# Performance work log

Hardware: AMD Instinct MI355X
Metric: run time of the kernel (lower is better)

Reference implementation:

```python
import jax, jax.numpy as jnp
import numpy as np

B, C, T = 4, 512, 4096
N2 = 32          # d_state // 2 complex modes
H = 2048         # hidden_channels
EPS = 1e-5


def setup_inputs() -> dict:
    key = jax.random.key(0)
    ks = jax.random.split(key, 8)
    dt_min, dt_max = 1e-3, 1e-1
    log_dt = jax.random.uniform(ks[1], (C,)) * (np.log(dt_max) - np.log(dt_min)) + np.log(dt_min)
    return {
        "x": jax.random.normal(ks[0], (B, C, T), jnp.float32),
        # ChannelwiseLayerNorm affine params
        "gamma": jnp.ones((C,), jnp.float32),
        "beta": jnp.zeros((C,), jnp.float32),
        # S4D kernel params (standard S4D-Lin init)
        "log_dt": log_dt.astype(jnp.float32),
        "C_re": jax.random.normal(ks[2], (C, N2), jnp.float32),
        "C_im": jax.random.normal(ks[3], (C, N2), jnp.float32),
        "log_A_real": jnp.log(0.5 * jnp.ones((C, N2), jnp.float32)),
        "A_imag": jnp.tile(jnp.pi * jnp.arange(N2, dtype=jnp.float32), (C, 1)),
        "D": jax.random.normal(ks[4], (C,), jnp.float32),
        # S4D output linear (Conv1d k=1 -> 2C, then GLU over channels)
        "Wo": jax.random.normal(ks[5], (2 * C, C), jnp.float32) / np.sqrt(C),
        "bo": jnp.zeros((2 * C,), jnp.float32),
        # FC MLP: Linear(C->H), PReLU(H), Linear(H->C)
        "W1": jax.random.normal(ks[6], (H, C), jnp.float32) / np.sqrt(C),
        "b1": jnp.zeros((H,), jnp.float32),
        "prelu_a": 0.25 * jnp.ones((H,), jnp.float32),
        "W2": jax.random.normal(ks[7], (C, H), jnp.float32) / np.sqrt(H),
        "b2": jnp.zeros((C,), jnp.float32),
    }


def reference(x, gamma, beta, log_dt, C_re, C_im, log_A_real, A_imag, D,
              Wo, bo, W1, b1, prelu_a, W2, b2):
    # ---- ChannelwiseLayerNorm over the channel dim of [B, C, T] ----
    mean = jnp.mean(x, axis=1, keepdims=True)
    var = jnp.var(x, axis=1, keepdims=True)
    u = gamma[None, :, None] * (x - mean) * jax.lax.rsqrt(var + EPS) + beta[None, :, None]

    # ---- S4D: diagonal SSM kernel via Vandermonde, applied by FFT conv ----
    L = x.shape[-1]
    dt = jnp.exp(log_dt)[:, None]                       # [C, 1]
    A = -jnp.exp(log_A_real) + 1j * A_imag              # [C, N2] complex diag
    dtA = A * dt                                        # [C, N2]
    Cd = (C_re + 1j * C_im) * (jnp.exp(dtA) - 1.0) / A  # discretized C (ZOH)
    vand = jnp.exp(dtA[..., None] * jnp.arange(L, dtype=jnp.float32))  # [C, N2, L]
    K = 2.0 * jnp.einsum('hn,hnl->hl', Cd, vand).real   # [C, L]

    k_f = jnp.fft.rfft(K, n=2 * L)                      # [C, L+1]
    u_f = jnp.fft.rfft(u, n=2 * L)                      # [B, C, L+1]
    y = jnp.fft.irfft(u_f * k_f, n=2 * L)[..., :L]      # causal conv
    y = y + u * D[None, :, None]                        # skip connection
    y = jax.nn.gelu(y, approximate=False)
    # output linear (1x1 conv to 2C) + GLU over channel dim
    z = jnp.einsum('oc,bct->bot', Wo, y) + bo[None, :, None]
    y = z[:, :C] * jax.nn.sigmoid(z[:, C:])             # [B, C, T]

    # ---- FC MLP with PReLU (per hidden channel) ----
    y = y.transpose(0, 2, 1)                            # [B, T, C]
    h = y @ W1.T + b1                                   # [B, T, H]
    h = jnp.where(h >= 0, h, prelu_a * h)
    y = h @ W2.T + b2                                   # [B, T, C]

    return x + y.transpose(0, 2, 1)                     # residual, [B, C, T]
```

## Files before the change

### kernel.cpp

```cpp
#include <hip/hip_runtime.h>
#include <math.h>

#define BB 4
#define CC 512
#define TT 4096
#define NN2 32
#define HH 2048

typedef __bf16 bf8v __attribute__((ext_vector_type(8)));
typedef __bf16 bf4v __attribute__((ext_vector_type(4)));
typedef float  f4v  __attribute__((ext_vector_type(4)));
typedef unsigned short u16x8 __attribute__((ext_vector_type(8)));

__device__ __forceinline__ void gload16(const void* g, void* l){
  __builtin_amdgcn_global_load_lds(
      (const __attribute__((address_space(1))) unsigned int*)g,
      (__attribute__((address_space(3))) unsigned int*)l, 16, 0, 0);
}
__device__ __forceinline__ float fast_gelu(float v){
  float x2 = v*v;
  float x  = 0.7978845608f*v*fmaf(0.044715f, x2, 1.0f);
  float t  = __expf(2.0f*x);
  return v - v*__builtin_amdgcn_rcpf(1.0f + t);
}
__device__ __forceinline__ float fast_sigmoid(float g){
  return __builtin_amdgcn_rcpf(1.0f + __expf(-g));
}
__device__ __forceinline__ unsigned short bfbits(float v){
  __bf16 h = (__bf16)v;
  return __builtin_bit_cast(unsigned short, h);
}

__global__ __launch_bounds__(256) void ln_kernel(
    const float* __restrict__ x, const float* __restrict__ gamma,
    const float* __restrict__ beta, __bf16* __restrict__ u)
{
  int tile = blockIdx.x & (TT/64 - 1);
  int b    = blockIdx.x >> 6;
  int tl = threadIdx.x & 63;
  int cg = threadIdx.x >> 6;
  int t = tile*64 + tl;
  const float* xp = x + (size_t)b*CC*TT + t;
  float s = 0.f, s2 = 0.f;
  #pragma unroll 4
  for (int c = cg*128; c < (cg+1)*128; ++c){
    float v = xp[(size_t)c*TT];
    s += v; s2 = fmaf(v, v, s2);
  }
  __shared__ float ls[4][64], ls2[4][64], mean_s[64], inv_s[64];
  ls[cg][tl] = s; ls2[cg][tl] = s2;
  __syncthreads();
  if (threadIdx.x < 64){
    float ss  = ls [0][tl]+ls [1][tl]+ls [2][tl]+ls [3][tl];
    float ss2 = ls2[0][tl]+ls2[1][tl]+ls2[2][tl]+ls2[3][tl];
    float mean = ss * (1.f/CC);
    float var  = ss2 * (1.f/CC) - mean*mean;
    mean_s[tl] = mean;
    inv_s[tl]  = rsqrtf(var + 1e-5f);
  }
  __syncthreads();
  float mean = mean_s[tl], inv = inv_s[tl];
  __bf16* up = u + (size_t)b*CC*TT + t;
  #pragma unroll 4
  for (int c = cg*128; c < (cg+1)*128; ++c){
    float v = xp[(size_t)c*TT];
    up[(size_t)c*TT] = (__bf16)fmaf(gamma[c]*inv, v - mean, beta[c]);
  }
}

__global__ __launch_bounds__(256) void build_mats(
    const float* __restrict__ log_dt, const float* __restrict__ C_re,
    const float* __restrict__ C_im, const float* __restrict__ log_A_real,
    const float* __restrict__ A_imag, const float* __restrict__ Dp,
    __bf16* __restrict__ Tt, __bf16* __restrict__ V, __bf16* __restrict__ B2)
{
  __shared__ float cpart[4][64][33];
  __shared__ float kk[4][65];
  const int wv = threadIdx.x >> 6, lane = threadIdx.x & 63;
  const int c = blockIdx.x*4 + wv;
  const int m = lane & 31;
  float dt = expf(log_dt[c]);
  float Ar = -expf(log_A_real[c*NN2+m]);
  float Ai = A_imag[c*NN2+m];
  float er = expf(Ar*dt);
  float sw_, cw_; sincosf(Ai*dt, &sw_, &cw_);
  float wre = er*cw_, wim = er*sw_;
  float nr = wre-1.f, ni = wim;
  float inv = 1.f/(Ar*Ar + Ai*Ai);
  float qr = (nr*Ar + ni*Ai)*inv;
  float qi = (ni*Ar - nr*Ai)*inv;
  float Cr = C_re[c*NN2+m], Ci = C_im[c*NN2+m];
  float okr =  2.f*(Cr*qr - Ci*qi);
  float oki = -2.f*(Cr*qi + Ci*qr);
  __bf16* Ttc = Tt + (size_t)c*4096;
  __bf16* Vc  = V  + (size_t)c*4096;
  __bf16* B2c = B2 + (size_t)c*4096;
  if (lane < 32){
    float pre = 1.f, pim = 0.f;
    for (int l = 0; l <= 64; ++l){
      if (l <= 63){
        Vc[(2*m)*64   + (63-l)] = (__bf16)pre;
        Vc[(2*m+1)*64 + (63-l)] = (__bf16)pim;
      }
      float cR = fmaf(okr, pre,  oki*pim);
      float cQ = fmaf(oki, pre, -okr*pim);
      if (l <= 63) cpart[wv][l][m] = cR;
      if (l >= 1){
        B2c[(l-1)*64 + 2*m]   = (__bf16)cR;
        B2c[(l-1)*64 + 2*m+1] = (__bf16)cQ;
      }
      float npre = wre*pre - wim*pim;
      float npim = wre*pim + wim*pre;
      pre = npre; pim = npim;
    }
  }
  __syncthreads();
  float s = 0.f;
  #pragma unroll
  for (int mm = 0; mm < 32; ++mm) s += cpart[wv][lane][mm];
  if (lane == 0) s += Dp[c];
  kk[wv][lane] = s;
  __syncthreads();
  const int n = lane;
  #pragma unroll
  for (int kb = 0; kb < 8; ++kb){
    u16x8 v;
    #pragma unroll
    for (int e = 0; e < 8; ++e){
      int k = kb*8 + e;
      v[e] = bfbits((n >= k) ? kk[wv][n-k] : 0.f);
    }
    *(u16x8*)&Ttc[n*64 + kb*8] = v;
  }
}

__global__ __launch_bounds__(128) void s4dm_kernel(
    const __bf16* __restrict__ u, const float* __restrict__ log_dt,
    const float* __restrict__ log_A_real, const float* __restrict__ A_imag,
    const __bf16* __restrict__ Tt, const __bf16* __restrict__ V,
    const __bf16* __restrict__ B2, __bf16* __restrict__ gout)
{
  __shared__ __align__(16) float gbuf[2][64][66];
  __shared__ __align__(16) unsigned short s0buf[2][64][72];
  const int wv = threadIdx.x >> 6, l = threadIdx.x & 63;
  const int lr = l & 15, q = l >> 4;
  const int seq = blockIdx.x*2 + wv;
  const int c = seq & (CC-1);
  const __bf16* Up  = u  + (size_t)seq*TT;
  const __bf16* Ttc = Tt + (size_t)c*4096;
  const __bf16* Vc  = V  + (size_t)c*4096;
  const __bf16* B2c = B2 + (size_t)c*4096;

  f4v acc[4][4];
  #pragma unroll
  for (int a=0;a<4;++a)
    #pragma unroll
    for (int b=0;b<4;++b)
      #pragma unroll
      for (int r=0;r<4;++r) acc[a][b][r] = 0.f;

  #pragma unroll
  for (int kw = 0; kw < 2; ++kw){
    bf8v af[4], bv[4];
    #pragma unroll
    for (int mt=0;mt<4;++mt)
      af[mt] = *(const bf8v*)(Up + (mt*16+lr)*64 + kw*32 + q*8);
    #pragma unroll
    for (int nt=0;nt<4;++nt)
      bv[nt] = *(const bf8v*)(Vc + (nt*16+lr)*64 + kw*32 + q*8);
    #pragma unroll
    for (int mt=0;mt<4;++mt)
      #pragma unroll
      for (int nt=0;nt<4;++nt)
        acc[mt][nt] = __builtin_amdgcn_mfma_f32_16x16x32_bf16(af[mt], bv[nt], acc[mt][nt], 0,0,0);
  }
  #pragma unroll
  for (int mt=0;mt<4;++mt)
    #pragma unroll
    for (int nt=0;nt<4;++nt)
      #pragma unroll
      for (int r=0;r<4;++r)
        gbuf[wv][mt*16 + q*4 + r][nt*16 + lr] = acc[mt][nt][r];
  __syncthreads();

  if (l < 32){
    const int m = l;
    float dt = expf(log_dt[c]);
    float Ar = -expf(log_A_real[c*NN2+m]);
    float Ai = A_imag[c*NN2+m];
    float er = expf(Ar*dt);
    float sw_, cw_; sincosf(Ai*dt, &sw_, &cw_);
    float wr_ = er*cw_, wi_ = er*sw_;
    #pragma unroll
    for (int sq2=0;sq2<6;++sq2){
      float a=wr_, b=wi_;
      wr_ = a*a - b*b; wi_ = 2.f*a*b;
    }
    float S0r=0.f, S0i=0.f;
    for (int j=0;j<64;++j){
      float gr = gbuf[wv][j][2*m], gi = gbuf[wv][j][2*m+1];
      s0buf[wv][j][2*m]   = bfbits(S0r);
      s0buf[wv][j][2*m+1] = bfbits(S0i);
      float nRe = fmaf(wr_, S0r, fmaf(-wi_, S0i, gr));
      float nIm = fmaf(wr_, S0i, fmaf( wi_, S0r, gi));
      S0r = nRe; S0i = nIm;
    }
  }
  __syncthreads();

  #pragma unroll
  for (int a=0;a<4;++a)
    #pragma unroll
    for (int b=0;b<4;++b)
      #pragma unroll
      for (int r=0;r<4;++r) acc[a][b][r] = 0.f;
  #pragma unroll
  for (int kw = 0; kw < 2; ++kw){
    bf8v af[4], bv[4];
    #pragma unroll
    for (int mt=0;mt<4;++mt)
      af[mt] = *(const bf8v*)(Up + (mt*16+lr)*64 + kw*32 + q*8);
    #pragma unroll
    for (int nt=0;nt<4;++nt)
      bv[nt] = *(const bf8v*)(Ttc + (nt*16+lr)*64 + kw*32 + q*8);
    #pragma unroll
    for (int mt=0;mt<4;++mt)
      #pragma unroll
      for (int nt=0;nt<4;++nt)
        acc[mt][nt] = __builtin_amdgcn_mfma_f32_16x16x32_bf16(af[mt], bv[nt], acc[mt][nt], 0,0,0);
  }
  #pragma unroll
  for (int kw = 0; kw < 2; ++kw){
    bf8v af[4], bv[4];
    #pragma unroll
    for (int mt=0;mt<4;++mt)
      af[mt] = *(const bf8v*)&s0buf[wv][mt*16+lr][kw*32 + q*8];
    #pragma unroll
    for (int nt=0;nt<4;++nt)
      bv[nt] = *(const bf8v*)(B2c + (nt*16+lr)*64 + kw*32 + q*8);
    #pragma unroll
    for (int mt=0;mt<4;++mt)
      #pragma unroll
      for (int nt=0;nt<4;++nt)
        acc[mt][nt] = __builtin_amdgcn_mfma_f32_16x16x32_bf16(af[mt], bv[nt], acc[mt][nt], 0,0,0);
  }
  __syncthreads();

  unsigned short (*ybuf)[72] = (unsigned short(*)[72])&gbuf[wv][0][0];
  #pragma unroll
  for (int mt=0;mt<4;++mt)
    #pragma unroll
    for (int nt=0;nt<4;++nt)
      #pragma unroll
      for (int r=0;r<4;++r)
        ybuf[mt*16 + q*4 + r][nt*16 + lr] = bfbits(fast_gelu(acc[mt][nt][r]));
  __syncthreads();
  u16x8* dst = (u16x8*)(gout + (size_t)seq*TT);
  for (int i = l; i < 512; i += 64){
    int row = i >> 3, cq = i & 7;
    dst[i] = *(const u16x8*)&ybuf[row][cq*8];
  }
}

__global__ __launch_bounds__(256) void tr_kernel(const __bf16* __restrict__ gin,
                                                 __bf16* __restrict__ gout)
{
  __shared__ __align__(16) unsigned short ts[64][72];
  int bt = blockIdx.x;
  int bc = blockIdx.y;
  int b  = blockIdx.z;
  int tid = threadIdx.x;
  const __bf16* gp = gin + ((size_t)b*CC + bc*64)*TT + (size_t)bt*64;
  for (int i = tid; i < 512; i += 256){
    int c = i >> 3, tq = i & 7;
    u16x8 v = *(const u16x8*)(gp + (size_t)c*TT + tq*8);
    #pragma unroll
    for (int s = 0; s < 8; ++s) ts[tq*8+s][c] = v[s];
  }
  __syncthreads();
  __bf16* op = gout + ((size_t)b*TT + bt*64)*CC + bc*64;
  for (int i = tid; i < 512; i += 256){
    int t = i >> 3, cq = i & 7;
    u16x8 v = *(const u16x8*)&ts[t][cq*8];
    *(u16x8*)(op + (size_t)t*CC + cq*8) = v;
  }
}

__global__ __launch_bounds__(256) void cvt_kernel(const float4* __restrict__ in,
                                                  bf4v* __restrict__ out, int n4)
{
  int i = blockIdx.x*256 + threadIdx.x;
  if (i < n4){
    float4 v = in[i];
    bf4v o; o[0]=(__bf16)v.x; o[1]=(__bf16)v.y; o[2]=(__bf16)v.z; o[3]=(__bf16)v.w;
    out[i] = o;
  }
}

template<int MODE>
__global__ __launch_bounds__(512, 2) void mm_kernel(
    const __bf16* __restrict__ Aw, const __bf16* __restrict__ Bt,
    const float* __restrict__ bias, const float* __restrict__ aux,
    void* __restrict__ outp)
{
  constexpr int K  = (MODE==2) ? 2048 : 512;
  constexpr int NT = K/32;
  constexpr int LOGGM = (MODE==1) ? 4 : 2;
  constexpr int GM = 1 << LOGGM;

  __shared__ __align__(16) __bf16 As[2*128*32];
  __shared__ __align__(16) __bf16 Bs[2*256*32];
  __shared__ __align__(16) __bf16 As2[(MODE==0)?2*128*32:8];

  const int bid = blockIdx.x;
  const int X = bid & 7, L = bid >> 3;
  const int m0 = (L & (GM-1)) * 128;
  const int n0 = (X*8 + (L >> LOGGM)) * 256;

  const int tid = threadIdx.x;
  const int l = tid & 63;
  const int lr = l & 15, kh = l >> 4;
  const int w = tid >> 6;
  const int wm = w >> 2, wn = w & 3;
  const int coff = (kh ^ ((lr ^ (lr >> 2)) & 3)) * 16;

  f4v acc[4][4];
  f4v acc2[(MODE==0)?4:1][(MODE==0)?4:1];
  #pragma unroll
  for (int a=0;a<4;++a)
    #pragma unroll
    for (int b=0;b<4;++b)
      #pragma unroll
      for (int r=0;r<4;++r) acc[a][b][r] = 0.f;
  if constexpr (MODE==0){
    #pragma unroll
    for (int a=0;a<4;++a)
      #pragma unroll
      for (int b=0;b<4;++b)
        #pragma unroll
        for (int r=0;r<4;++r) acc2[a][b][r] = 0.f;
  }

  const char* pA  = (const char*)Aw;
  const char* pA2 = (const char*)(Aw + (size_t)CC*K);
  const char* pB  = (const char*)Bt;

  auto stage = [&](int d, int kt){
    {
      int cch = tid;
      int row = cch >> 2;
      int kb = ((cch & 3) ^ ((row ^ (row >> 2)) & 3)) * 16;
      gload16(pA + ((size_t)(m0+row)*K + kt*32)*2 + kb, (char*)As + d*8192 + cch*16);
      if constexpr (MODE==0)
        gload16(pA2 + ((size_t)(m0+row)*K + kt*32)*2 + kb, (char*)As2 + d*8192 + cch*16);
    }
    #pragma unroll
    for (int i=0;i<2;++i){
      int cch = i*512 + tid;
      int row = cch >> 2;
      int kb = ((cch & 3) ^ ((row ^ (row >> 2)) & 3)) * 16;
      gload16(pB + ((size_t)(n0+row)*K + kt*32)*2 + kb, (char*)Bs + d*16384 + cch*16);
    }
  };

  auto compute = [&](int d){
    bf8v af[4], bv4[4];
    #pragma unroll
    for (int mi=0;mi<4;++mi){
      int row = wm*64 + mi*16 + lr;
      af[mi] = *(const bf8v*)((const char*)As + d*8192 + row*64 + coff);
    }
    #pragma unroll
    for (int ni=0;ni<4;++ni){
      int row = wn*64 + ni*16 + lr;
      bv4[ni] = *(const bf8v*)((const char*)Bs + d*16384 + row*64 + coff);
    }
    if constexpr (MODE==0){
      bf8v af2[4];
      #pragma unroll
      for (int mi=0;mi<4;++mi){
        int row = wm*64 + mi*16 + lr;
        af2[mi] = *(const bf8v*)((const char*)As2 + d*8192 + row*64 + coff);
      }
      #pragma unroll
      for (int mi=0;mi<4;++mi)
        #pragma unroll
        for (int ni=0;ni<4;++ni){
          acc [mi][ni] = __builtin_amdgcn_mfma_f32_16x16x32_bf16(af [mi], bv4[ni], acc [mi][ni], 0,0,0);
          acc2[mi][ni] = __builtin_amdgcn_mfma_f32_16x16x32_bf16(af2[mi], bv4[ni], acc2[mi][ni], 0,0,0);
        }
    } else {
      #pragma unroll
      for (int mi=0;mi<4;++mi)
        #pragma unroll
        for (int ni=0;ni<4;++ni)
          acc[mi][ni] = __builtin_amdgcn_mfma_f32_16x16x32_bf16(af[mi], bv4[ni], acc[mi][ni], 0,0,0);
    }
  };

  stage(0, 0);
  __syncthreads();
  int cur = 0;
  #pragma unroll 1
  for (int kt = 1; kt < NT; ++kt){
    stage(cur ^ 1, kt);
    compute(cur);
    __syncthreads();
    cur ^= 1;
  }
  compute(cur);

  if constexpr (MODE==0 || MODE==1){
    const int COUT = (MODE==0) ? CC : HH;
    __bf16* O = (__bf16*)outp;
    #pragma unroll
    for (int mi=0;mi<4;++mi){
      int m = m0 + wm*64 + mi*16 + kh*4;
      float4 bi = *(const float4*)&bias[m];
      float bia[4] = {bi.x, bi.y, bi.z, bi.w};
      float gta[4], paa[4];
      if constexpr (MODE==0){
        float4 bg = *(const float4*)&bias[CC + m];
        gta[0]=bg.x; gta[1]=bg.y; gta[2]=bg.z; gta[3]=bg.w;
      } else {
        float4 pa = *(const float4*)&aux[m];
        paa[0]=pa.x; paa[1]=pa.y; paa[2]=pa.z; paa[3]=pa.w;
      }
      #pragma unroll
      for (int ni=0;ni<4;++ni){
        int tok = n0 + wn*64 + ni*16 + lr;
        bf4v o;
        #pragma unroll
        for (int r=0;r<4;++r){
          float v = acc[mi][ni][r] + bia[r];
          if constexpr (MODE==0){
            float gate = acc2[mi][ni][r] + gta[r];
            v = v * fast_sigmoid(gate);
          } else {
            v = (v >= 0.f) ? v : paa[r]*v;
          }
          o[r] = (__bf16)v;
        }
        *(bf4v*)&O[(size_t)tok*COUT + m] = o;
      }
    }
  } else {
    float* O = (float*)outp;
    #pragma unroll
    for (int mi=0;mi<4;++mi){
      int chb = m0 + wm*64 + mi*16 + kh*4;
      float4 bi = *(const float4*)&bias[chb];
      float bia[4] = {bi.x, bi.y, bi.z, bi.w};
      #pragma unroll
      for (int ni=0;ni<4;++ni){
        int tok = n0 + wn*64 + ni*16 + lr;
        int b = tok >> 12, t = tok & 4095;
        size_t rb = ((size_t)(b*CC + chb))*TT + t;
        #pragma unroll
        for (int r=0;r<4;++r)
          O[rb + (size_t)r*TT] = acc[mi][ni][r] + bia[r] + aux[rb + (size_t)r*TT];
      }
    }
  }
}

extern "C" void kernel_launch(void* const* d_in, const int* in_sizes, int n_in,
                              void* d_out, int out_size, void* d_ws, size_t ws_size,
                              hipStream_t stream)
{
  const float* x          = (const float*)d_in[0];
  const float* gamma      = (const float*)d_in[1];
  const float* beta       = (const float*)d_in[2];
  const float* log_dt     = (const float*)d_in[3];
  const float* C_re       = (const float*)d_in[4];
  const float* C_im       = (const float*)d_in[5];
  const float* log_A_real = (const float*)d_in[6];
  const float* A_imag     = (const float*)d_in[7];
  const float* Dp         = (const float*)d_in[8];
  const float* Wo         = (const float*)d_in[9];
  const float* bo         = (const float*)d_in[10];
  const float* W1         = (const float*)d_in[11];
  const float* b1         = (const float*)d_in[12];
  const float* prelu_a    = (const float*)d_in[13];
  const float* W2         = (const float*)d_in[14];
  const float* b2         = (const float*)d_in[15];
  float* out = (float*)d_out;

  char* base = (char*)d_ws;
  const size_t SEGB = (size_t)BB*CC*TT*2;
  __bf16* u_bf  = (__bf16*)(base);
  __bf16* glu   = (__bf16*)(base);
  __bf16* g_cm  = (__bf16*)(base + SEGB);
  __bf16* g_tm  = (__bf16*)(base + 2*SEGB);
  __bf16* h     = (__bf16*)(base + SEGB);
  __bf16* Tt_all = (__bf16*)(base + 2*SEGB);
  __bf16* V_all  = Tt_all + (size_t)CC*4096;
  __bf16* B2_all = V_all  + (size_t)CC*4096;
  __bf16* Wo_bf = (__bf16*)(base + 5*SEGB);
  __bf16* W1_bf = Wo_bf + (size_t)2*CC*CC;
  __bf16* W2_bf = W1_bf + (size_t)HH*CC;

  cvt_kernel<<<dim3((2*CC*CC/4 + 255)/256), 256, 0, stream>>>((const float4*)Wo, (bf4v*)Wo_bf, 2*CC*CC/4);
  cvt_kernel<<<dim3((HH*CC/4 + 255)/256), 256, 0, stream>>>((const float4*)W1, (bf4v*)W1_bf, HH*CC/4);
  cvt_kernel<<<dim3((CC*HH/4 + 255)/256), 256, 0, stream>>>((const float4*)W2, (bf4v*)W2_bf, CC*HH/4);

  build_mats<<<dim3(CC/4), 256, 0, stream>>>(log_dt, C_re, C_im, log_A_real,
                                             A_imag, Dp, Tt_all, V_all, B2_all);
  ln_kernel<<<dim3(BB*(TT/64)), 256, 0, stream>>>(x, gamma, beta, u_bf);
  s4dm_kernel<<<dim3((BB*CC)/2), 128, 0, stream>>>(u_bf, log_dt, log_A_real, A_imag,
                                                   Tt_all, V_all, B2_all, g_cm);
  tr_kernel<<<dim3(TT/64, CC/64, BB), 256, 0, stream>>>(g_cm, g_tm);

  mm_kernel<0><<<dim3(4*64),  512, 0, stream>>>(Wo_bf, g_tm, bo, nullptr, (void*)glu);
  mm_kernel<1><<<dim3(16*64), 512, 0, stream>>>(W1_bf, glu, b1, prelu_a, (void*)h);
  mm_kernel<2><<<dim3(4*64),  512, 0, stream>>>(W2_bf, h, b2, x, (void*)out);
}
```

Before: 220.1 us.

## Deepen GEMM prefetch to a four-stage LDS ring with vmcnt waits

Replaces the double-buffered LDS staging in the three GEMM modes with a four-slot ring that keeps three k-tiles of global-to-LDS loads in flight. It waits on exact vmcnt counts plus raw barriers instead of draining with __syncthreads, with the aim of hiding memory latency behind MFMA work. It also raises wave priority around the MFMA block and uses nontemporal stores for the hidden activations and the final residual output, plus nontemporal loads of the residual input. The shared-memory footprint doubles (up to 128KB in the gated mode), which likely cuts resident blocks per CU from two to one and reduces latency hiding across blocks.

Measured after the change: 297.5 us. +35.2%, slower.

```diff
diff --git a/kernel.cpp b/kernel.cpp
--- a/kernel.cpp
+++ b/kernel.cpp
@@ -307,10 +307,11 @@
   constexpr int NT = K/32;
   constexpr int LOGGM = (MODE==1) ? 4 : 2;
   constexpr int GM = 1 << LOGGM;
-
-  __shared__ __align__(16) __bf16 As[2*128*32];
-  __shared__ __align__(16) __bf16 Bs[2*256*32];
-  __shared__ __align__(16) __bf16 As2[(MODE==0)?2*128*32:8];
+  constexpr int LPS = (MODE==0) ? 4 : 3;
+
+  __shared__ __align__(16) __bf16 As[4*128*32];
+  __shared__ __align__(16) __bf16 Bs[4*256*32];
+  __shared__ __align__(16) __bf16 As2[(MODE==0)?4*128*32:8];
 
   const int bid = blockIdx.x;
   const int X = bid & 7, L = bid >> 3;
@@ -363,6 +364,13 @@
     }
   };
 
+  auto vwait = [&](int ahead){
+    if (ahead >= 3)      asm volatile("s_waitcnt vmcnt(%0)" :: "n"(3*LPS) : "memory");
+    else if (ahead == 2) asm volatile("s_waitcnt vmcnt(%0)" :: "n"(2*LPS) : "memory");
+    else if (ahead == 1) asm volatile("s_waitcnt vmcnt(%0)" :: "n"(1*LPS) : "memory");
+    else                 asm volatile("s_waitcnt vmcnt(0)" ::: "memory");
+  };
+
   auto compute = [&](int d){
     bf8v af[4], bv4[4];
     #pragma unroll
@@ -382,6 +390,7 @@
         int row = wm*64 + mi*16 + lr;
         af2[mi] = *(const bf8v*)((const char*)As2 + d*8192 + row*64 + coff);
       }
+      __builtin_amdgcn_s_setprio(1);
       #pragma unroll
       for (int mi=0;mi<4;++mi)
         #pragma unroll
@@ -389,26 +398,28 @@
           acc [mi][ni] = __builtin_amdgcn_mfma_f32_16x16x32_bf16(af [mi], bv4[ni], acc [mi][ni], 0,0,0);
           acc2[mi][ni] = __builtin_amdgcn_mfma_f32_16x16x32_bf16(af2[mi], bv4[ni], acc2[mi][ni], 0,0,0);
         }
+      __builtin_amdgcn_s_setprio(0);
     } else {
+      __builtin_amdgcn_s_setprio(1);
       #pragma unroll
       for (int mi=0;mi<4;++mi)
         #pragma unroll
         for (int ni=0;ni<4;++ni)
           acc[mi][ni] = __builtin_amdgcn_mfma_f32_16x16x32_bf16(af[mi], bv4[ni], acc[mi][ni], 0,0,0);
+      __builtin_amdgcn_s_setprio(0);
     }
   };
 
-  stage(0, 0);
-  __syncthreads();
-  int cur = 0;
+  stage(0, 0); stage(1, 1); stage(2, 2);
   #pragma unroll 1
-  for (int kt = 1; kt < NT; ++kt){
-    stage(cur ^ 1, kt);
-    compute(cur);
-    __syncthreads();
-    cur ^= 1;
-  }
-  compute(cur);
+  for (int kt = 0; kt < NT; ++kt){
+    if (kt + 3 < NT) stage((kt+3)&3, kt+3);
+    int ahead = NT-1-kt; ahead = (ahead > 3) ? 3 : ahead;
+    vwait(ahead);
+    __builtin_amdgcn_s_barrier();
+    compute(kt & 3);
+    __builtin_amdgcn_s_barrier();
+  }
 
   if constexpr (MODE==0 || MODE==1){
     const int COUT = (MODE==0) ? CC : HH;
@@ -441,7 +452,10 @@
           }
           o[r] = (__bf16)v;
         }
-        *(bf4v*)&O[(size_t)tok*COUT + m] = o;
+        if constexpr (MODE==0)
+          *(bf4v*)&O[(size_t)tok*COUT + m] = o;
+        else
+          __builtin_nontemporal_store(o, (bf4v*)&O[(size_t)tok*COUT + m]);
       }
     }
   } else {
@@ -457,8 +471,11 @@
         int b = tok >> 12, t = tok & 4095;
         size_t rb = ((size_t)(b*CC + chb))*TT + t;
         #pragma unroll
-        for (int r=0;r<4;++r)
-          O[rb + (size_t)r*TT] = acc[mi][ni][r] + bia[r] + aux[rb + (size_t)r*TT];
+        for (int r=0;r<4;++r){
+          float xv = __builtin_nontemporal_load(&aux[rb + (size_t)r*TT]);
+          __builtin_nontemporal_store(acc[mi][ni][r] + bia[r] + xv,
+                                      &O[rb + (size_t)r*TT]);
+        }
       }
     }
   }
```
